# Performance work log

Measured on AMD Instinct MI355X. Metric: run time of the kernel, lower is better.

Reference implementation:

```python
import jax, jax.numpy as jnp
import numpy as np

VOCAB = 4096
B, L = 4, 2048


def setup_inputs() -> dict:
    key = jax.random.key(0)
    k_idx, k_m, k_w1, k_b1, k_w2, k_b2 = jax.random.split(key, 6)
    V = VOCAB
    idx = jax.random.randint(k_idx, (B, L), 0, V)
    morphisms_logits = jax.random.normal(k_m, (V, V), dtype=jnp.float32)
    # Linear layers: V -> 2V -> V (scaled init for numerical sanity)
    W1 = jax.random.normal(k_w1, (V, 2 * V), dtype=jnp.float32) * 0.02
    b1 = jnp.zeros((2 * V,), dtype=jnp.float32)
    W2 = jax.random.normal(k_w2, (2 * V, V), dtype=jnp.float32) * 0.02
    b2 = jnp.zeros((V,), dtype=jnp.float32)
    return {"idx": idx, "morphisms_logits": morphisms_logits,
            "W1": W1, "b1": b1, "W2": W2, "b2": b2}


def reference(idx, morphisms_logits, W1, b1, W2, b2):
    # YonedaEmbedding: row-gather from sigmoid(logits)  -> x [B, L, V]
    R = jax.nn.sigmoid(morphisms_logits)
    x = R[idx]
    # Causal mean pooling: tril-mask matmul / row counts == cumulative mean.
    # O(L*D) prefix-sum form, mathematically identical to the O(L^2*D) matmul.
    seq_len = x.shape[1]
    counts = jnp.arange(1, seq_len + 1, dtype=x.dtype)[:, None]  # [L, 1]
    context = jnp.cumsum(x, axis=1) / counts                      # [B, L, V]
    # FFN: Linear(V, 2V) -> GELU (exact, matches torch default) -> Linear(2V, V)
    h = jax.nn.gelu(context @ W1 + b1, approximate=False)
    logits = h @ W2 + b2
    return logits
```

## Files before the change

### kernel.cpp

```cpp
#include <hip/hip_runtime.h>
#include <hip/hip_bf16.h>

#define VOCAB 4096
#define BB 4
#define LL 2048
#define SEG 16
#define SEGL 128

typedef __hip_bfloat16 bf16;
typedef __bf16 bf16x8 __attribute__((ext_vector_type(8)));
typedef float f32x4 __attribute__((ext_vector_type(4)));

__device__ __forceinline__ void gload16(const void* g, void* l) {
  __builtin_amdgcn_global_load_lds(
      (const __attribute__((address_space(1))) unsigned int*)g,
      (__attribute__((address_space(3))) unsigned int*)l, 16, 0, 0);
}

__device__ __forceinline__ bf16x8 as_bf(f32x4 v) {
  union { f32x4 f; bf16x8 b; } u;
  u.f = v;
  return u.b;
}

__global__ void transpose_f32_bf16(const float* __restrict__ in,
                                   bf16* __restrict__ out, int K, int N) {
  __shared__ float tile[32][33];
  int bx = blockIdx.x;
  int by = blockIdx.y;
  int x = bx * 32 + threadIdx.x;
#pragma unroll
  for (int i = threadIdx.y; i < 32; i += 8)
    tile[i][threadIdx.x] = in[(size_t)(by * 32 + i) * N + x];
  __syncthreads();
  int k = by * 32 + threadIdx.x;
#pragma unroll
  for (int i = threadIdx.y; i < 32; i += 8)
    out[(size_t)(bx * 32 + i) * K + k] = __float2bfloat16(tile[threadIdx.x][i]);
}

__global__ void ctx_partial(const int* __restrict__ idx,
                            const float* __restrict__ Mlog,
                            float* __restrict__ segsum) {
  int b = blockIdx.x / (16 * SEG);
  int rem = blockIdx.x % (16 * SEG);
  int chunk = rem / SEG;
  int s = rem % SEG;
  int col = chunk * 256 + threadIdx.x;
  __shared__ int sidx[SEGL];
  if (threadIdx.x < SEGL)
    sidx[threadIdx.x] = idx[b * LL + s * SEGL + threadIdx.x];
  __syncthreads();
  const float* base = Mlog + col;
  float a0 = 0.f, a1 = 0.f, a2 = 0.f, a3 = 0.f;
#pragma unroll 4
  for (int t = 0; t < SEGL; t += 4) {
    float v0 = base[(size_t)sidx[t + 0] * VOCAB];
    float v1 = base[(size_t)sidx[t + 1] * VOCAB];
    float v2 = base[(size_t)sidx[t + 2] * VOCAB];
    float v3 = base[(size_t)sidx[t + 3] * VOCAB];
    a0 += 1.f / (1.f + __expf(-v0));
    a1 += 1.f / (1.f + __expf(-v1));
    a2 += 1.f / (1.f + __expf(-v2));
    a3 += 1.f / (1.f + __expf(-v3));
  }
  segsum[(size_t)blockIdx.x * 256 + threadIdx.x] = (a0 + a1) + (a2 + a3);
}

__global__ void ctx_final(const int* __restrict__ idx,
                          const float* __restrict__ Mlog,
                          const float* __restrict__ segsum,
                          bf16* __restrict__ ctx) {
  int b = blockIdx.x / (16 * SEG);
  int rem = blockIdx.x % (16 * SEG);
  int chunk = rem / SEG;
  int s = rem % SEG;
  int col = chunk * 256 + threadIdx.x;
  __shared__ int sidx[SEGL];
  if (threadIdx.x < SEGL)
    sidx[threadIdx.x] = idx[b * LL + s * SEGL + threadIdx.x];
  __syncthreads();
  const float* ss = segsum + (size_t)((b * 16 + chunk) * SEG) * 256 + threadIdx.x;
  float acc = 0.f;
  for (int s2 = 0; s2 < s; ++s2) acc += ss[(size_t)s2 * 256];
  const float* base = Mlog + col;
  bf16* outp = ctx + ((size_t)b * LL + (size_t)s * SEGL) * VOCAB + col;
#pragma unroll 8
  for (int t = 0; t < SEGL; ++t) {
    float v = base[(size_t)sidx[t] * VOCAB];
    acc += 1.f / (1.f + __expf(-v));
    float inv = __fdividef(1.f, (float)(s * SEGL + t + 1));
    outp[(size_t)t * VOCAB] = __float2bfloat16(acc * inv);
  }
}


#define BAR() asm volatile("s_barrier" ::: "memory")
#define LGKM0() asm volatile("s_waitcnt lgkmcnt(0)" ::: "memory")
#define VMW(n_) asm volatile("s_waitcnt vmcnt(" #n_ ")" ::: "memory")
#define SB0() __builtin_amdgcn_sched_barrier(0)
#define P1() __builtin_amdgcn_s_setprio(1)
#define P0() __builtin_amdgcn_s_setprio(0)

#define STG_A(t_, h_, b_)                                           \
  {                                                                 \
    const bf16* s_ = Asrc + (size_t)(h_)*128 * K + (size_t)(t_)*64; \
    bf16* d_ = sm + (b_)*32768 + (h_)*8192 + wave * 512;            \
    gload16(s_, d_);                                                \
    gload16(s_ + rowK64, d_ + 4096);                                \
  }
#define STG_B(t_, h_, b_)                                           \
  {                                                                 \
    const bf16* s_ = Bsrc + (size_t)(h_)*128 * K + (size_t)(t_)*64; \
    bf16* d_ = sm + (b_)*32768 + 16384 + (h_)*8192 + wave * 512;    \
    gload16(s_, d_);                                                \
    gload16(s_ + rowK64, d_ + 4096);                                \
  }

#define RD1(dst_, base_, off_)                       \
  asm volatile("ds_read_b128 %0, %1 offset:%2"       \
               : "=v"(dst_)                          \
               : "v"(base_), "i"(off_)               \
               : "memory")

#define RD_A(b0_, b1_, mh_)                    \
  RD1(af[0][0], b0_, (mh_)*16384 + 0);         \
  RD1(af[0][1], b1_, (mh_)*16384 + 0);         \
  RD1(af[1][0], b0_, (mh_)*16384 + 2048);      \
  RD1(af[1][1], b1_, (mh_)*16384 + 2048);      \
  RD1(af[2][0], b0_, (mh_)*16384 + 4096);      \
  RD1(af[2][1], b1_, (mh_)*16384 + 4096);      \
  RD1(af[3][0], b0_, (mh_)*16384 + 6144);      \
  RD1(af[3][1], b1_, (mh_)*16384 + 6144);

#define RD_B(dst_, b0_, b1_, nh_)              \
  RD1(dst_[0][0], b0_, (nh_)*16384 + 0);       \
  RD1(dst_[0][1], b1_, (nh_)*16384 + 0);       \
  RD1(dst_[1][0], b0_, (nh_)*16384 + 2048);    \
  RD1(dst_[1][1], b1_, (nh_)*16384 + 2048);

#define MQ(mh_, nh_, B_)                                                     \
  _Pragma("unroll") for (int i_ = 0; i_ < 4; ++i_)                           \
      _Pragma("unroll") for (int j_ = 0; j_ < 2; ++j_) {                     \
    f32x4& c_ = acc[(mh_)*4 + i_][(nh_)*2 + j_];                             \
    c_ = __builtin_amdgcn_mfma_f32_16x16x32_bf16(as_bf(af[i_][0]),           \
                                                 as_bf(B_[j_][0]), c_, 0, 0, \
                                                 0);                         \
    c_ = __builtin_amdgcn_mfma_f32_16x16x32_bf16(as_bf(af[i_][1]),           \
                                                 as_bf(B_[j_][1]), c_, 0, 0, \
                                                 0);                         \
  }

#define TILE_BODY(T_, p_, aK0_, aK1_, bK0_, bK1_, bn0_, bn1_, Bc_, Bn_) \
  {                                                                     \
          \
    if ((T_) + 1 < NT) { VMW(4); } else { VMW(0); }                     \
    BAR();                                                              \
            \
    RD_A(aK0_, aK1_, 0);                                                \
    if ((T_) + 1 < NT) STG_A((T_) + 1, 0, (p_) ^ 1);                    \
    LGKM0();                                                            \
    SB0();                                                              \
    P1(); MQ(0, 0, Bc_); P0();                                          \
        \
    RD_B(Bn_, bK0_, bK1_, 1);                                           \
    if ((T_) + 1 < NT) STG_A((T_) + 1, 1, (p_) ^ 1);                    \
    LGKM0();                                                            \
    SB0();                                                              \
    P1(); MQ(0, 1, Bn_); P0();                                          \
                         \
    VMW(6);                                                             \
    BAR();                                                              \
             \
    RD_A(aK0_, aK1_, 1);                                                \
    if ((T_) + 2 < NT) STG_B((T_) + 2, 0, (p_));                        \
    LGKM0();                                                            \
    SB0();                                                              \
    P1(); MQ(1, 1, Bn_); P0();                                          \
               \
    if ((T_) + 1 < NT) RD_B(Bn_, bn0_, bn1_, 0);                        \
    if ((T_) + 2 < NT) STG_B((T_) + 2, 1, (p_));                        \
    P1(); MQ(1, 0, Bc_); P0();                                          \
  }

template <int EPI>
__global__ __launch_bounds__(512) void gemm256(const bf16* __restrict__ A,
                                               const bf16* __restrict__ Bt,
                                               const float* __restrict__ bias,
                                               void* __restrict__ outv, int M,
                                               int N, int K) {
  __shared__ __align__(16) bf16 sm[65536];
  const int tid = threadIdx.x;
  const int wave = tid >> 6;
  const int lane = tid & 63;
  const int nwg = gridDim.x;
  const int bid = blockIdx.x;
  const int swz = (bid & 7) * (nwg >> 3) + (bid >> 3);
  const int gn = N >> 8;
  const int bm0 = (swz / gn) << 8;
  const int bn0 = (swz % gn) << 8;
  const int wm64 = (wave >> 2) << 6;
  const int wn32 = (wave & 3) << 5;
  const int rsel = lane & 15;
  const int ksel = lane >> 4;
  const int xorv = rsel & 7;

  const int r0 = tid >> 3;
  const int kc0 = (tid & 7) ^ (r0 & 7);
  const bf16* Asrc = A + (size_t)(bm0 + r0) * K + kc0 * 8;
  const bf16* Bsrc = Bt + (size_t)(bn0 + r0) * K + kc0 * 8;
  const size_t rowK64 = (size_t)64 * K;
  const int NT = K >> 6;

  const unsigned smbase =
      (unsigned)(unsigned long long)(__attribute__((address_space(3)))
                                     bf16*)sm;
  const unsigned kT0 = (unsigned)((ksel ^ xorv) << 4);
  const unsigned kT1 = (unsigned)(((ksel + 4) ^ xorv) << 4);
  const unsigned aRow = (unsigned)((wm64 + rsel) * 128);
  const unsigned bRow = (unsigned)((wn32 + rsel) * 128);
  const unsigned a00 = smbase + aRow + kT0;
  const unsigned a10 = smbase + aRow + kT1;
  const unsigned b00 = smbase + 32768u + bRow + kT0;
  const unsigned b10 = smbase + 32768u + bRow + kT1;
  const unsigned a01 = a00 + 65536u, a11 = a10 + 65536u;
  const unsigned b01 = b00 + 65536u, b11 = b10 + 65536u;

  f32x4 acc[8][4];
#pragma unroll
  for (int i = 0; i < 8; ++i)
#pragma unroll
    for (int j = 0; j < 4; ++j) acc[i][j] = (f32x4){0.f, 0.f, 0.f, 0.f};

  f32x4 af[4][2], bX[2][2], bY[2][2];

  STG_A(0, 0, 0);
  STG_A(0, 1, 0);
  STG_B(0, 0, 0);
  STG_B(0, 1, 0);
  STG_B(1, 0, 1);
  STG_B(1, 1, 1);
  VMW(4);
  BAR();
  RD_B(bX, b00, b10, 0);

  for (int t = 0; t < NT; t += 2) {
    TILE_BODY(t, 0, a00, a10, b00, b10, b01, b11, bX, bY);
    TILE_BODY(t + 1, 1, a01, a11, b01, b11, b00, b10, bY, bX);
  }

  const int cl = lane & 15;
  const int rg = lane >> 4;
#pragma unroll
  for (int m = 0; m < 8; ++m) {
    int grow = bm0 + ((m >> 2) << 7) + wm64 + ((m & 3) << 4) + rg * 4;
#pragma unroll
    for (int n = 0; n < 4; ++n) {
      int col = bn0 + ((n >> 1) << 7) + wn32 + ((n & 1) << 4) + cl;
      float bv = bias[col];
#pragma unroll
      for (int r = 0; r < 4; ++r) {
        size_t o = (size_t)(grow + r) * N + col;
        float v = acc[m][n][r] + bv;
        if (EPI == 0) {
          float g = 0.5f * v * (1.f + erff(v * 0.70710678118654752f));
          ((bf16*)outv)[o] = __float2bfloat16(g);
        } else {
          ((float*)outv)[o] = v;
        }
      }
    }
  }
}

extern "C" void kernel_launch(void* const* d_in, const int* in_sizes, int n_in,
                              void* d_out, int out_size, void* d_ws,
                              size_t ws_size, hipStream_t stream) {
  const int* idx = (const int*)d_in[0];
  const float* Mlog = (const float*)d_in[1];
  const float* W1 = (const float*)d_in[2];
  const float* b1 = (const float*)d_in[3];
  const float* W2 = (const float*)d_in[4];
  const float* b2 = (const float*)d_in[5];
  float* out = (float*)d_out;

  char* ws = (char*)d_ws;
  const size_t MB64 = 64ull << 20;
  bf16* ctx = (bf16*)ws;
  bf16* W2t = (bf16*)ws;
  bf16* W1t = (bf16*)(ws + MB64);
  bf16* h = (bf16*)(ws + 2 * MB64);
  float* segsum = (float*)h;
  (void)ws_size;

  dim3 tb(32, 8);
  transpose_f32_bf16<<<dim3(8192 / 32, 4096 / 32), tb, 0, stream>>>(W1, W1t,
                                                                    4096, 8192);
  ctx_partial<<<BB * 16 * SEG, 256, 0, stream>>>(idx, Mlog, segsum);
  ctx_final<<<BB * 16 * SEG, 256, 0, stream>>>(idx, Mlog, segsum, ctx);
  gemm256<0><<<(8192 / 256) * (8192 / 256), 512, 0, stream>>>(
      ctx, W1t, b1, h, 8192, 8192, 4096);
  transpose_f32_bf16<<<dim3(4096 / 32, 8192 / 32), tb, 0, stream>>>(W2, W2t,
                                                                    8192, 4096);
  gemm256<1><<<(8192 / 256) * (4096 / 256), 512, 0, stream>>>(
      h, W2t, b2, out, 8192, 4096, 8192);
}
```

Measured before the change: 987.7 us.

## Precompute sigmoid(M)@W1 then gather and prefix-average projected rows

Uses linearity: the cumulative mean of gathered rows times W1 equals the cumulative mean of gathered rows of sigmoid(M)@W1. The first GEMM now runs over the 4096-row vocabulary table instead of the 8192 token rows. Bias, prefix averaging and GELU are fused into the gather/scan kernels that write h directly. This halves first-GEMM FLOPs. In exchange the scan now reads and writes 8192-wide rows and projected values are rounded to bf16 before averaging, which changes the error profile.

```diff
diff --git a/kernel.cpp b/kernel.cpp
--- a/kernel.cpp
+++ b/kernel.cpp
@@ -6,6 +6,7 @@
 #define LL 2048
 #define SEG 16
 #define SEGL 128
+#define CH 16
 
 typedef __hip_bfloat16 bf16;
 typedef __bf16 bf16x8 __attribute__((ext_vector_type(8)));
@@ -39,58 +40,77 @@
     out[(size_t)(bx * 32 + i) * K + k] = __float2bfloat16(tile[threadIdx.x][i]);
 }
 
-__global__ void ctx_partial(const int* __restrict__ idx,
-                            const float* __restrict__ Mlog,
-                            float* __restrict__ segsum) {
-  int b = blockIdx.x / (16 * SEG);
-  int rem = blockIdx.x % (16 * SEG);
+__global__ void sigmoid_bf16(const float* __restrict__ in,
+                             bf16* __restrict__ out) {
+  size_t i = ((size_t)blockIdx.x * 256 + threadIdx.x) * 4;
+  float4 v = *(const float4*)(in + i);
+  bf16 tmp[4];
+  tmp[0] = __float2bfloat16(1.f / (1.f + __expf(-v.x)));
+  tmp[1] = __float2bfloat16(1.f / (1.f + __expf(-v.y)));
+  tmp[2] = __float2bfloat16(1.f / (1.f + __expf(-v.z)));
+  tmp[3] = __float2bfloat16(1.f / (1.f + __expf(-v.w)));
+  *(ushort4*)(out + i) = *(ushort4*)tmp;
+}
+
+__global__ void psumA(const int* __restrict__ idx, const bf16* __restrict__ P,
+                      float* __restrict__ segsum) {
+  int b = blockIdx.x / (CH * SEG);
+  int rem = blockIdx.x % (CH * SEG);
   int chunk = rem / SEG;
   int s = rem % SEG;
-  int col = chunk * 256 + threadIdx.x;
+  int col = chunk * 512 + threadIdx.x * 2;
   __shared__ int sidx[SEGL];
   if (threadIdx.x < SEGL)
     sidx[threadIdx.x] = idx[b * LL + s * SEGL + threadIdx.x];
   __syncthreads();
-  const float* base = Mlog + col;
-  float a0 = 0.f, a1 = 0.f, a2 = 0.f, a3 = 0.f;
-#pragma unroll 4
-  for (int t = 0; t < SEGL; t += 4) {
-    float v0 = base[(size_t)sidx[t + 0] * VOCAB];
-    float v1 = base[(size_t)sidx[t + 1] * VOCAB];
-    float v2 = base[(size_t)sidx[t + 2] * VOCAB];
-    float v3 = base[(size_t)sidx[t + 3] * VOCAB];
-    a0 += 1.f / (1.f + __expf(-v0));
-    a1 += 1.f / (1.f + __expf(-v1));
-    a2 += 1.f / (1.f + __expf(-v2));
-    a3 += 1.f / (1.f + __expf(-v3));
-  }
-  segsum[(size_t)blockIdx.x * 256 + threadIdx.x] = (a0 + a1) + (a2 + a3);
-}
-
-__global__ void ctx_final(const int* __restrict__ idx,
-                          const float* __restrict__ Mlog,
-                          const float* __restrict__ segsum,
-                          bf16* __restrict__ ctx) {
-  int b = blockIdx.x / (16 * SEG);
-  int rem = blockIdx.x % (16 * SEG);
+  const __hip_bfloat162* base = (const __hip_bfloat162*)P + (col >> 1);
+  float a0 = 0.f, a1 = 0.f;
+#pragma unroll 8
+  for (int t = 0; t < SEGL; ++t) {
+    __hip_bfloat162 v = base[(size_t)sidx[t] * 4096];
+    a0 += __bfloat162float(v.x);
+    a1 += __bfloat162float(v.y);
+  }
+  *((float2*)(segsum + (size_t)blockIdx.x * 512) + threadIdx.x) =
+      make_float2(a0, a1);
+}
+
+__global__ void psumB(const int* __restrict__ idx, const bf16* __restrict__ P,
+                      const float* __restrict__ segsum,
+                      const float* __restrict__ b1, bf16* __restrict__ h) {
+  int b = blockIdx.x / (CH * SEG);
+  int rem = blockIdx.x % (CH * SEG);
   int chunk = rem / SEG;
   int s = rem % SEG;
-  int col = chunk * 256 + threadIdx.x;
+  int col = chunk * 512 + threadIdx.x * 2;
   __shared__ int sidx[SEGL];
   if (threadIdx.x < SEGL)
     sidx[threadIdx.x] = idx[b * LL + s * SEGL + threadIdx.x];
   __syncthreads();
-  const float* ss = segsum + (size_t)((b * 16 + chunk) * SEG) * 256 + threadIdx.x;
-  float acc = 0.f;
-  for (int s2 = 0; s2 < s; ++s2) acc += ss[(size_t)s2 * 256];
-  const float* base = Mlog + col;
-  bf16* outp = ctx + ((size_t)b * LL + (size_t)s * SEGL) * VOCAB + col;
-#pragma unroll 8
+  const float2* ss =
+      (const float2*)(segsum + (size_t)((b * CH + chunk) * SEG) * 512) +
+      threadIdx.x;
+  float a0 = 0.f, a1 = 0.f;
+  for (int s2 = 0; s2 < s; ++s2) {
+    float2 t = ss[(size_t)s2 * 256];
+    a0 += t.x;
+    a1 += t.y;
+  }
+  float2 bias = *(const float2*)(b1 + col);
+  const __hip_bfloat162* base = (const __hip_bfloat162*)P + (col >> 1);
+  bf16* outp = h + ((size_t)b * LL + (size_t)s * SEGL) * 8192 + col;
+#pragma unroll 4
   for (int t = 0; t < SEGL; ++t) {
-    float v = base[(size_t)sidx[t] * VOCAB];
-    acc += 1.f / (1.f + __expf(-v));
+    __hip_bfloat162 v = base[(size_t)sidx[t] * 4096];
+    a0 += __bfloat162float(v.x);
+    a1 += __bfloat162float(v.y);
     float inv = __fdividef(1.f, (float)(s * SEGL + t + 1));
-    outp[(size_t)t * VOCAB] = __float2bfloat16(acc * inv);
+    float u0 = a0 * inv + bias.x;
+    float u1 = a1 * inv + bias.y;
+    __hip_bfloat162 o;
+    o.x = __float2bfloat16(0.5f * u0 * (1.f + erff(u0 * 0.70710678118654752f)));
+    o.y = __float2bfloat16(0.5f * u1 * (1.f + erff(u1 * 0.70710678118654752f)));
+    *(__hip_bfloat162*)(outp + (size_t)t * 8192) = o;
   }
 }
 
@@ -153,31 +173,25 @@
 
 #define TILE_BODY(T_, p_, aK0_, aK1_, bK0_, bK1_, bn0_, bn1_, Bc_, Bn_) \
   {                                                                     \
-          \
     if ((T_) + 1 < NT) { VMW(4); } else { VMW(0); }                     \
     BAR();                                                              \
-            \
     RD_A(aK0_, aK1_, 0);                                                \
     if ((T_) + 1 < NT) STG_A((T_) + 1, 0, (p_) ^ 1);                    \
     LGKM0();                                                            \
     SB0();                                                              \
     P1(); MQ(0, 0, Bc_); P0();                                          \
-        \
     RD_B(Bn_, bK0_, bK1_, 1);                                           \
     if ((T_) + 1 < NT) STG_A((T_) + 1, 1, (p_) ^ 1);                    \
     LGKM0();                                                            \
     SB0();                                                              \
     P1(); MQ(0, 1, Bn_); P0();                                          \
-                         \
     VMW(6);                                                             \
     BAR();                                                              \
-             \
     RD_A(aK0_, aK1_, 1);                                                \
     if ((T_) + 2 < NT) STG_B((T_) + 2, 0, (p_));                        \
     LGKM0();                                                            \
     SB0();                                                              \
     P1(); MQ(1, 1, Bn_); P0();                                          \
-               \
     if ((T_) + 1 < NT) RD_B(Bn_, bn0_, bn1_, 0);                        \
     if ((T_) + 2 < NT) STG_B((T_) + 2, 1, (p_));                        \
     P1(); MQ(1, 0, Bc_); P0();                                          \
@@ -257,16 +271,14 @@
 #pragma unroll
     for (int n = 0; n < 4; ++n) {
       int col = bn0 + ((n >> 1) << 7) + wn32 + ((n & 1) << 4) + cl;
-      float bv = bias[col];
+      float bv = (EPI == 1) ? bias[col] : 0.f;
 #pragma unroll
       for (int r = 0; r < 4; ++r) {
         size_t o = (size_t)(grow + r) * N + col;
-        float v = acc[m][n][r] + bv;
-        if (EPI == 0) {
-          float g = 0.5f * v * (1.f + erff(v * 0.70710678118654752f));
-          ((bf16*)outv)[o] = __float2bfloat16(g);
+        if (EPI == 1) {
+          ((float*)outv)[o] = acc[m][n][r] + bv;
         } else {
-          ((float*)outv)[o] = v;
+          ((bf16*)outv)[o] = __float2bfloat16(acc[m][n][r]);
         }
       }
     }
@@ -285,21 +297,23 @@
   float* out = (float*)d_out;
 
   char* ws = (char*)d_ws;
-  const size_t MB64 = 64ull << 20;
-  bf16* ctx = (bf16*)ws;
+  const size_t MB = 1ull << 20;
+  bf16* W1t = (bf16*)ws;
+  float* segsum = (float*)ws;
   bf16* W2t = (bf16*)ws;
-  bf16* W1t = (bf16*)(ws + MB64);
-  bf16* h = (bf16*)(ws + 2 * MB64);
-  float* segsum = (float*)h;
+  bf16* P = (bf16*)(ws + 64 * MB);
+  bf16* h = (bf16*)(ws + 128 * MB);
+  bf16* R = (bf16*)(ws + 224 * MB);
   (void)ws_size;
 
   dim3 tb(32, 8);
   transpose_f32_bf16<<<dim3(8192 / 32, 4096 / 32), tb, 0, stream>>>(W1, W1t,
                                                                     4096, 8192);
-  ctx_partial<<<BB * 16 * SEG, 256, 0, stream>>>(idx, Mlog, segsum);
-  ctx_final<<<BB * 16 * SEG, 256, 0, stream>>>(idx, Mlog, segsum, ctx);
-  gemm256<0><<<(8192 / 256) * (8192 / 256), 512, 0, stream>>>(
-      ctx, W1t, b1, h, 8192, 8192, 4096);
+  sigmoid_bf16<<<(VOCAB * VOCAB) / 1024, 256, 0, stream>>>(Mlog, R);
+  gemm256<2><<<(4096 / 256) * (8192 / 256), 512, 0, stream>>>(
+      R, W1t, b1, P, 4096, 8192, 4096);
+  psumA<<<BB * CH * SEG, 256, 0, stream>>>(idx, P, segsum);
+  psumB<<<BB * CH * SEG, 256, 0, stream>>>(idx, P, segsum, b1, h);
   transpose_f32_bf16<<<dim3(4096 / 32, 8192 / 32), tb, 0, stream>>>(W2, W2t,
                                                                     8192, 4096);
   gemm256<1><<<(8192 / 256) * (4096 / 256), 512, 0, stream>>>(
```

New measurement: 823.5 us. 16.6% less time.
